# Kernel tuning notes

Hardware: AMD Instinct MI355X
Metric: run time of the kernel (lower is better)

The kernel has to match this reference:

```python
import jax, jax.numpy as jnp
import numpy as np
from jax import lax

BN_EPS = 1e-5

def _bn(x, g, b):
    # eval-mode BatchNorm with default running stats (mean=0, var=1)
    sh = (1, -1) + (1,) * (x.ndim - 2)
    return x * (g / jnp.sqrt(1.0 + BN_EPS)).reshape(sh) + b.reshape(sh)

def _simam(x, lam=1e-4):
    axes = tuple(range(2, x.ndim))
    mu = x.mean(axis=axes, keepdims=True)
    d2 = (x - mu) ** 2
    var = d2.mean(axis=axes, keepdims=True)
    e = d2 / (2.0 * var + 1e-12) + lam
    return jax.nn.sigmoid(1.0 / (e + 1e-12)) * x

def _dwconv1d(x, w, pad, groups):
    return lax.conv_general_dilated(
        x, w, (1,), [(pad, pad)],
        dimension_numbers=('NCH', 'OIH', 'NCH'),
        feature_group_count=groups)

def _adaptive_pool_matrix(t_in, t_out):
    # torch AdaptiveAvgPool1d: window i = [floor(i*t_in/t_out), ceil((i+1)*t_in/t_out))
    M = np.zeros((t_in, t_out), dtype=np.float32)
    for i in range(t_out):
        s = (i * t_in) // t_out
        e = -(-((i + 1) * t_in) // t_out)
        M[s:e, i] = 1.0 / (e - s)
    return jnp.asarray(M)

def _deform_conv1d(x, w, ow, ob):
    # depthwise deformable conv1d, padding='valid'; grid_sample bilinear,
    # zeros padding, align_corners=True -> pure 1D bilinear gather at pos.
    B, C, T = x.shape
    K = w.shape[1]
    T_out = T - K + 1
    off = _dwconv1d(x, ow, 0, C) + ob[None, :, None]        # (B, C*K, T_out)
    off = off.reshape(B, C, K, T_out)
    pos = (jnp.arange(T_out, dtype=x.dtype)[None, None, None, :]
           + jnp.arange(K, dtype=x.dtype)[None, None, :, None] + off)
    i0f = jnp.floor(pos)
    f = pos - i0f
    i0 = i0f.astype(jnp.int32)
    xb = jnp.broadcast_to(x[:, :, None, :], (B, C, K, T))
    def gather(idx):
        valid = (idx >= 0) & (idx < T)
        v = jnp.take_along_axis(xb, jnp.clip(idx, 0, T - 1), axis=3)
        return jnp.where(valid, v, 0.0)
    samp = gather(i0) * (1.0 - f) + gather(i0 + 1) * f      # (B,C,K,T_out)
    return jnp.einsum('bckt,ck->bct', samp, w)

def _branch(x, sw, g1, b1, tw, g2, b2):
    # spatial depthwise conv (kernel covers full channel axis) -> (B,5,T)
    h = jnp.einsum('bcht,ch->bct', x, sw)
    h = _simam(jax.nn.elu(_bn(h, g1, b1)))
    h = _dwconv1d(h, tw, tw.shape[-1] // 2, h.shape[1])     # temporal depthwise, same length
    return _simam(jax.nn.elu(_bn(h, g2, b2)))

def setup_inputs() -> dict:
    key = jax.random.key(0)
    ks = iter(jax.random.split(key, 48))
    B, C_in, T, n_class = 256, 22, 1000, 4
    k1, k2, k3 = 15, 31, 63  # _odd(round(fs*{0.06,0.12,0.25})), fs=250
    def rn(shape, scale=0.1):
        return scale * jax.random.normal(next(ks), shape, dtype=jnp.float32)
    inp = {'x': jax.random.normal(next(ks), (B, 1, C_in, T), dtype=jnp.float32),
           'stem_w': rn((15, 1, 2, 3)),
           'stem_g': 1.0 + rn((15,)), 'stem_b': rn((15,))}
    for i, kt in zip((1, 2, 3), (k1, k2, k3)):
        inp[f'b{i}_sw'] = rn((5, C_in))
        inp[f'b{i}_g1'] = 1.0 + rn((5,)); inp[f'b{i}_b1'] = rn((5,))
        inp[f'b{i}_tw'] = rn((5, 1, kt))
        inp[f'b{i}_g2'] = 1.0 + rn((5,)); inp[f'b{i}_b2'] = rn((5,))
    inp['pw_w'] = rn((5, 15))
    inp['pw_g'] = 1.0 + rn((5,)); inp['pw_b'] = rn((5,))
    inp['d1_w'] = rn((5, 5));  inp['d1_ow'] = rn((25, 1, 5), 0.02);  inp['d1_ob'] = jnp.zeros((25,), jnp.float32)
    inp['d2_w'] = rn((5, 10)); inp['d2_ow'] = rn((50, 1, 10), 0.02); inp['d2_ob'] = jnp.zeros((50,), jnp.float32)
    inp['fc_w'] = rn((n_class, 5 * 25)); inp['fc_b'] = rn((n_class,))
    return inp

def reference(x, stem_w, stem_g, stem_b,
              b1_sw, b1_g1, b1_b1, b1_tw, b1_g2, b1_b2,
              b2_sw, b2_g1, b2_b1, b2_tw, b2_g2, b2_b2,
              b3_sw, b3_g1, b3_b1, b3_tw, b3_g2, b3_b2,
              pw_w, pw_g, pw_b,
              d1_w, d1_ow, d1_ob, d2_w, d2_ow, d2_ob,
              fc_w, fc_b):
    # stem: conv2d k=(2,3) 'same' (torch pads extra on the right for even k)
    h = lax.conv_general_dilated(x, stem_w, (1, 1), [(0, 1), (1, 1)],
                                 dimension_numbers=('NCHW', 'OIHW', 'NCHW'))
    h = jax.nn.elu(_bn(h, stem_g, stem_b))                  # (B,15,22,T); dropout = eval no-op
    o1 = _branch(h[:, 0:5],  b1_sw, b1_g1, b1_b1, b1_tw, b1_g2, b1_b2)
    o2 = _branch(h[:, 5:10], b2_sw, b2_g1, b2_b1, b2_tw, b2_g2, b2_b2)
    o3 = _branch(h[:, 10:15], b3_sw, b3_g1, b3_b1, b3_tw, b3_g2, b3_b2)
    hc = jnp.concatenate([o1, o2, o3], axis=1)              # (B,15,T)
    hc = jnp.einsum('bct,to->bco', hc, _adaptive_pool_matrix(hc.shape[-1], 40))
    hc = jnp.einsum('bct,oc->bot', hc, pw_w)                # 1x1 pointwise
    hc = _simam(jax.nn.elu(_bn(hc, pw_g, pw_b)))            # (B,5,40)
    hc = _deform_conv1d(hc, d1_w, d1_ow, d1_ob)             # (B,5,36)
    hc = _deform_conv1d(hc, d2_w, d2_ow, d2_ob)             # (B,5,27)
    hc = jnp.einsum('bct,to->bco', hc, _adaptive_pool_matrix(hc.shape[-1], 25))
    return hc.reshape(hc.shape[0], -1) @ fc_w.T + fc_b      # (B,n_class)
```

## Files before the change

kernel.cpp:

```cpp
#include <hip/hip_runtime.h>
#include <math.h>

#define BNS 0.99999500003749972f

__device__ __forceinline__ float eluf(float v) {
    return v > 0.f ? v : (__expf(v) - 1.f);
}
__device__ __forceinline__ float sigmf(float u) {
    return 1.f / (1.f + __expf(-u));
}
__device__ __forceinline__ float sgpr(float v) {
    return __int_as_float(__builtin_amdgcn_readfirstlane(__float_as_int(v)));
}

#define PSTR 1024
#define PADZ 32
#define ZLEN 1120

__device__ __forceinline__ void block_reduce2(float& s1, float& s2, float* red) {
#pragma unroll
    for (int m = 32; m > 0; m >>= 1) {
        s1 += __shfl_xor(s1, m, 64);
        s2 += __shfl_xor(s2, m, 64);
    }
    const int wid = threadIdx.x >> 6, lane = threadIdx.x & 63;
    if (lane == 0) { red[wid * 2] = s1; red[wid * 2 + 1] = s2; }
    __syncthreads();
    s1 = red[0] + red[2] + red[4] + red[6];
    s2 = red[1] + red[3] + red[5] + red[7];
}

__global__ __launch_bounds__(256) void k_stem(
    const float* __restrict__ x,
    const float* __restrict__ stem_w,
    const float* __restrict__ stem_g, const float* __restrict__ stem_b,
    const float* __restrict__ sw1, const float* __restrict__ sw2, const float* __restrict__ sw3,
    float* __restrict__ pre)
{
    const int tid = threadIdx.x;
    const int lane = tid & 63;
    const int g = blockIdx.y;
    const int b = blockIdx.z;
    const float* xb = x + b * 22000;

    const float* swp = (g == 0 ? sw1 : g == 1 ? sw2 : sw3);
    float wrow[5];
#pragma unroll
    for (int c = 0; c < 5; ++c)
        wrow[c] = (lane < 22) ? swp[c * 22 + lane] : 0.f;

    if (tid >= 250) return;
    const int t0 = blockIdx.x * 500 + tid * 2;

    float w[5][6], bs[5];
#pragma unroll
    for (int c = 0; c < 5; ++c) {
        const int C = g * 5 + c;
        const float gsc = sgpr(stem_g[C]) * BNS;
#pragma unroll
        for (int j = 0; j < 6; ++j) w[c][j] = sgpr(stem_w[C * 6 + j]) * gsc;
        bs[c] = sgpr(stem_b[C]);
    }

    const bool sel0 = (t0 == 0), sel2 = (t0 == 998);
    const int base = sel0 ? 0 : (sel2 ? 996 : t0 - 1);

    float acc0[5] = {0.f, 0.f, 0.f, 0.f, 0.f};
    float acc1[5] = {0.f, 0.f, 0.f, 0.f, 0.f};

    #define LOADW(rp, w0, w1, w2, w3)                                   \
    {                                                                   \
        const float4 v = *reinterpret_cast<const float4*>((rp) + base); \
        w0 = sel0 ? 0.f : (sel2 ? v.y : v.x);                           \
        w1 = sel0 ? v.x : (sel2 ? v.z : v.y);                           \
        w2 = sel0 ? v.y : (sel2 ? v.w : v.z);                           \
        w3 = sel2 ? 0.f : (sel0 ? v.z : v.w);                           \
    }

    float c0, c1, c2, c3, n0, n1, n2, n3;
    LOADW(xb, c0, c1, c2, c3)
    for (int i = 0; i < 22; ++i) {
        if (i < 21) {
            LOADW(xb + (i + 1) * 1000, n0, n1, n2, n3)
        } else {
            n0 = n1 = n2 = n3 = 0.f;
        }
#pragma unroll
        for (int c = 0; c < 5; ++c) {
            const float sv = __shfl(wrow[c], i, 64);
            float v0 = fmaf(w[c][0], c0, fmaf(w[c][1], c1, fmaf(w[c][2], c2,
                       fmaf(w[c][3], n0, fmaf(w[c][4], n1, fmaf(w[c][5], n2, bs[c]))))));
            float v1 = fmaf(w[c][0], c1, fmaf(w[c][1], c2, fmaf(w[c][2], c3,
                       fmaf(w[c][3], n1, fmaf(w[c][4], n2, fmaf(w[c][5], n3, bs[c]))))));
            acc0[c] += eluf(v0) * sv;
            acc1[c] += eluf(v1) * sv;
        }
        c0 = n0; c1 = n1; c2 = n2; c3 = n3;
    }
    #undef LOADW

    float* prow0 = pre + (b * 15 + g * 5) * PSTR + t0;
#pragma unroll
    for (int c = 0; c < 5; ++c) {
        float2 o; o.x = acc0[c]; o.y = acc1[c];
        *reinterpret_cast<float2*>(prow0 + c * PSTR) = o;
    }
}

template<int K>
__device__ __forceinline__ void branch_block(
    const float* __restrict__ row,
    float g1s, float b1v,
    float wreg,
    float g2s, float b2v,
    float* __restrict__ zrow,
    float* __restrict__ red,
    float* __restrict__ out40)
{
    const int tid = threadIdx.x;
    const int t0 = tid * 4;
    const bool act = tid < 250;

    if (tid < PADZ) zrow[tid] = 0.f;
    if (tid >= 32 && tid < 120) zrow[PADZ + 1000 + (tid - 32)] = 0.f;

    float y0 = 0.f, y1 = 0.f, y2 = 0.f, y3 = 0.f, s1 = 0.f, s2 = 0.f;
    if (act) {
        const float4 v = *reinterpret_cast<const float4*>(row + t0);
        y0 = eluf(v.x * g1s + b1v);
        y1 = eluf(v.y * g1s + b1v);
        y2 = eluf(v.z * g1s + b1v);
        y3 = eluf(v.w * g1s + b1v);
        s1 = y0 + y1 + y2 + y3;
        s2 = y0 * y0 + y1 * y1 + y2 * y2 + y3 * y3;
    }
    block_reduce2(s1, s2, red);
    {
        const float mu = s1 * 1e-3f;
        const float var = s2 * 1e-3f - mu * mu;
        const float iv = 1.f / (2.f * var + 1e-12f);
        if (act) {
            float d;
            float4 z;
            d = y0 - mu; z.x = sigmf(1.f / (d * d * iv + 1e-4f + 1e-12f)) * y0;
            d = y1 - mu; z.y = sigmf(1.f / (d * d * iv + 1e-4f + 1e-12f)) * y1;
            d = y2 - mu; z.z = sigmf(1.f / (d * d * iv + 1e-4f + 1e-12f)) * y2;
            d = y3 - mu; z.w = sigmf(1.f / (d * d * iv + 1e-4f + 1e-12f)) * y3;
            *reinterpret_cast<float4*>(&zrow[PADZ + t0]) = z;
        }
    }
    __syncthreads();

    float a0 = 0.f, a1 = 0.f, a2 = 0.f, a3 = 0.f;
    if (act) {
        const int A = PADZ + t0 - (K / 2) - 1;
        float W[20];
#pragma unroll
        for (int q = 0; q < 5; ++q)
            *reinterpret_cast<float4*>(&W[q * 4]) = *reinterpret_cast<const float4*>(&zrow[A + q * 4]);

#pragma unroll
        for (int cb = 0; cb < K; cb += 16) {
            float P[16];
            if (cb + 16 < K) {
#pragma unroll
                for (int q = 0; q < 4; ++q)
                    *reinterpret_cast<float4*>(&P[q * 4]) =
                        *reinterpret_cast<const float4*>(&zrow[A + cb + 20 + q * 4]);
            }
            const int DD = (K - cb < 16) ? (K - cb) : 16;
#pragma unroll
            for (int dd = 0; dd < DD; ++dd) {
                const float wv = __shfl(wreg, cb + dd, 64);
                a0 += W[dd + 1] * wv;
                a1 += W[dd + 2] * wv;
                a2 += W[dd + 3] * wv;
                a3 += W[dd + 4] * wv;
            }
            if (cb + 16 < K) {
#pragma unroll
                for (int q = 0; q < 4; ++q) W[q] = W[16 + q];
#pragma unroll
                for (int q = 0; q < 16; ++q) W[4 + q] = P[q];
            }
        }
    }

    float u0 = 0.f, u1 = 0.f, u2 = 0.f, u3 = 0.f;
    s1 = 0.f; s2 = 0.f;
    if (act) {
        u0 = eluf(a0 * g2s + b2v);
        u1 = eluf(a1 * g2s + b2v);
        u2 = eluf(a2 * g2s + b2v);
        u3 = eluf(a3 * g2s + b2v);
        s1 = u0 + u1 + u2 + u3;
        s2 = u0 * u0 + u1 * u1 + u2 * u2 + u3 * u3;
    }
    block_reduce2(s1, s2, red);
    {
        const float mu = s1 * 1e-3f;
        const float var = s2 * 1e-3f - mu * mu;
        const float iv = 1.f / (2.f * var + 1e-12f);
        if (act) {
            float d;
            float4 z;
            d = u0 - mu; z.x = sigmf(1.f / (d * d * iv + 1e-4f + 1e-12f)) * u0;
            d = u1 - mu; z.y = sigmf(1.f / (d * d * iv + 1e-4f + 1e-12f)) * u1;
            d = u2 - mu; z.z = sigmf(1.f / (d * d * iv + 1e-4f + 1e-12f)) * u2;
            d = u3 - mu; z.w = sigmf(1.f / (d * d * iv + 1e-4f + 1e-12f)) * u3;
            *reinterpret_cast<float4*>(&zrow[PADZ + t0]) = z;
        }
    }
    __syncthreads();

    if (tid < 40) {
        float s = 0.f;
#pragma unroll
        for (int q = 0; q < 25; ++q) s += zrow[PADZ + tid * 25 + q];
        out40[tid] = s * (1.f / 25.f);
    }
}

__global__ __launch_bounds__(256) void k_branch(
    const float* __restrict__ pre,
    const float* __restrict__ g1a, const float* __restrict__ b1a,
    const float* __restrict__ tw1,
    const float* __restrict__ g2a, const float* __restrict__ b2a,
    const float* __restrict__ g1b, const float* __restrict__ b1b,
    const float* __restrict__ tw2,
    const float* __restrict__ g2b, const float* __restrict__ b2b,
    const float* __restrict__ g1c, const float* __restrict__ b1c,
    const float* __restrict__ tw3,
    const float* __restrict__ g2c, const float* __restrict__ b2c,
    float* __restrict__ pooled)
{
    __shared__ float zrow[ZLEN];
    __shared__ float red[8];

    const int row_id = blockIdx.x;
    const int C = row_id % 15;
    const int br = C / 5, c = C % 5;
    const int lane = threadIdx.x & 63;

    const float* row = pre + (size_t)row_id * PSTR;
    float* out40 = pooled + row_id * 40;

    if (br == 0) {
        const float wreg = (lane < 15) ? tw1[c * 15 + lane] : 0.f;
        branch_block<15>(row, g1a[c] * BNS, b1a[c], wreg, g2a[c] * BNS, b2a[c], zrow, red, out40);
    } else if (br == 1) {
        const float wreg = (lane < 31) ? tw2[c * 31 + lane] : 0.f;
        branch_block<31>(row, g1b[c] * BNS, b1b[c], wreg, g2b[c] * BNS, b2b[c], zrow, red, out40);
    } else {
        const float wreg = (lane < 63) ? tw3[c * 63 + lane] : 0.f;
        branch_block<63>(row, g1c[c] * BNS, b1c[c], wreg, g2c[c] * BNS, b2c[c], zrow, red, out40);
    }
}

__global__ __launch_bounds__(128) void k_head(
    const float* __restrict__ pooled,
    const float* __restrict__ pw_w, const float* __restrict__ pw_g, const float* __restrict__ pw_b,
    const float* __restrict__ d1_w, const float* __restrict__ d1_ow, const float* __restrict__ d1_ob,
    const float* __restrict__ d2_w, const float* __restrict__ d2_ow, const float* __restrict__ d2_ob,
    const float* __restrict__ fc_w, const float* __restrict__ fc_b,
    float* __restrict__ out)
{
    __shared__ float P[600];
    __shared__ float A[200];
    __shared__ float Bv[200];
    __shared__ float C1[180];
    __shared__ float C2[135];
    __shared__ float D[125];
    __shared__ float mu5[5], iv5[5];

    const int b = blockIdx.x, tid = threadIdx.x;

    for (int i = tid; i < 600; i += 128) P[i] = pooled[b * 600 + i];
    __syncthreads();

    for (int i = tid; i < 200; i += 128) {
        int o = i / 40, t = i % 40;
        float s = 0.f;
        for (int cc = 0; cc < 15; ++cc) s += P[cc * 40 + t] * pw_w[o * 15 + cc];
        float v = s * (pw_g[o] * BNS) + pw_b[o];
        A[i] = eluf(v);
    }
    __syncthreads();

    if (tid < 5) {
        float s = 0.f;
        for (int t = 0; t < 40; ++t) s += A[tid * 40 + t];
        float mu = s * (1.f / 40.f);
        float v2 = 0.f;
        for (int t = 0; t < 40; ++t) { float d = A[tid * 40 + t] - mu; v2 += d * d; }
        mu5[tid] = mu;
        iv5[tid] = 1.f / (2.f * (v2 * (1.f / 40.f)) + 1e-12f);
    }
    __syncthreads();

    for (int i = tid; i < 200; i += 128) {
        int o = i / 40;
        float a = A[i];
        float d = a - mu5[o];
        float e = d * d * iv5[o] + 1e-4f;
        Bv[i] = sigmf(1.f / (e + 1e-12f)) * a;
    }
    __syncthreads();

    for (int i = tid; i < 180; i += 128) {
        int cc = i / 36, t = i % 36;
        float o = 0.f;
        for (int k = 0; k < 5; ++k) {
            float off = d1_ob[cc * 5 + k];
            for (int d = 0; d < 5; ++d) off += Bv[cc * 40 + t + d] * d1_ow[(cc * 5 + k) * 5 + d];
            float pos = (float)(t + k) + off;
            float fl = floorf(pos);
            float f = pos - fl;
            int i0 = (int)fl;
            float v0 = (i0 >= 0 && i0 < 40) ? Bv[cc * 40 + i0] : 0.f;
            float v1 = (i0 + 1 >= 0 && i0 + 1 < 40) ? Bv[cc * 40 + i0 + 1] : 0.f;
            o += (v0 * (1.f - f) + v1 * f) * d1_w[cc * 5 + k];
        }
        C1[i] = o;
    }
    __syncthreads();

    for (int i = tid; i < 135; i += 128) {
        int cc = i / 27, t = i % 27;
        float o = 0.f;
        for (int k = 0; k < 10; ++k) {
            float off = d2_ob[cc * 10 + k];
            for (int d = 0; d < 10; ++d) off += C1[cc * 36 + t + d] * d2_ow[(cc * 10 + k) * 10 + d];
            float pos = (float)(t + k) + off;
            float fl = floorf(pos);
            float f = pos - fl;
            int i0 = (int)fl;
            float v0 = (i0 >= 0 && i0 < 36) ? C1[cc * 36 + i0] : 0.f;
            float v1 = (i0 + 1 >= 0 && i0 + 1 < 36) ? C1[cc * 36 + i0 + 1] : 0.f;
            o += (v0 * (1.f - f) + v1 * f) * d2_w[cc * 10 + k];
        }
        C2[i] = o;
    }
    __syncthreads();

    for (int i = tid; i < 125; i += 128) {
        int cc = i / 25, j = i % 25;
        int s0 = (j * 27) / 25;
        int e0 = ((j + 1) * 27 + 24) / 25;
        float s = 0.f;
        for (int q = s0; q < e0; ++q) s += C2[cc * 27 + q];
        D[i] = s / (float)(e0 - s0);
    }
    __syncthreads();

    if (tid < 64) {
        float part0 = 0.f, part1 = 0.f, part2 = 0.f, part3 = 0.f;
        for (int i = tid; i < 125; i += 64) {
            const float dv = D[i];
            part0 += dv * fc_w[0 * 125 + i];
            part1 += dv * fc_w[1 * 125 + i];
            part2 += dv * fc_w[2 * 125 + i];
            part3 += dv * fc_w[3 * 125 + i];
        }
#pragma unroll
        for (int m = 32; m > 0; m >>= 1) {
            part0 += __shfl_xor(part0, m, 64);
            part1 += __shfl_xor(part1, m, 64);
            part2 += __shfl_xor(part2, m, 64);
            part3 += __shfl_xor(part3, m, 64);
        }
        if (tid == 0) {
            out[b * 4 + 0] = part0 + fc_b[0];
            out[b * 4 + 1] = part1 + fc_b[1];
            out[b * 4 + 2] = part2 + fc_b[2];
            out[b * 4 + 3] = part3 + fc_b[3];
        }
    }
}

extern "C" void kernel_launch(void* const* d_in, const int* in_sizes, int n_in,
                              void* d_out, int out_size, void* d_ws, size_t ws_size,
                              hipStream_t stream) {
    const float* x      = (const float*)d_in[0];
    const float* stem_w = (const float*)d_in[1];
    const float* stem_g = (const float*)d_in[2];
    const float* stem_b = (const float*)d_in[3];
    const float* b1_sw = (const float*)d_in[4];
    const float* b1_g1 = (const float*)d_in[5];
    const float* b1_b1 = (const float*)d_in[6];
    const float* b1_tw = (const float*)d_in[7];
    const float* b1_g2 = (const float*)d_in[8];
    const float* b1_b2 = (const float*)d_in[9];
    const float* b2_sw = (const float*)d_in[10];
    const float* b2_g1 = (const float*)d_in[11];
    const float* b2_b1 = (const float*)d_in[12];
    const float* b2_tw = (const float*)d_in[13];
    const float* b2_g2 = (const float*)d_in[14];
    const float* b2_b2 = (const float*)d_in[15];
    const float* b3_sw = (const float*)d_in[16];
    const float* b3_g1 = (const float*)d_in[17];
    const float* b3_b1 = (const float*)d_in[18];
    const float* b3_tw = (const float*)d_in[19];
    const float* b3_g2 = (const float*)d_in[20];
    const float* b3_b2 = (const float*)d_in[21];
    const float* pw_w  = (const float*)d_in[22];
    const float* pw_g  = (const float*)d_in[23];
    const float* pw_b  = (const float*)d_in[24];
    const float* d1_w  = (const float*)d_in[25];
    const float* d1_ow = (const float*)d_in[26];
    const float* d1_ob = (const float*)d_in[27];
    const float* d2_w  = (const float*)d_in[28];
    const float* d2_ow = (const float*)d_in[29];
    const float* d2_ob = (const float*)d_in[30];
    const float* fc_w  = (const float*)d_in[31];
    const float* fc_b  = (const float*)d_in[32];

    float* pre    = (float*)d_ws;
    float* pooled = (float*)((char*)d_ws + (size_t)256 * 15 * PSTR * 4);

    k_stem<<<dim3(2, 3, 256), 256, 0, stream>>>(
        x, stem_w, stem_g, stem_b, b1_sw, b2_sw, b3_sw, pre);

    k_branch<<<3840, 256, 0, stream>>>(
        pre,
        b1_g1, b1_b1, b1_tw, b1_g2, b1_b2,
        b2_g1, b2_b1, b2_tw, b2_g2, b2_b2,
        b3_g1, b3_b1, b3_tw, b3_g2, b3_b2,
        pooled);

    k_head<<<256, 128, 0, stream>>>(
        pooled, pw_w, pw_g, pw_b,
        d1_w, d1_ow, d1_ob, d2_w, d2_ow, d2_ob,
        fc_w, fc_b, (float*)d_out);
}
```

Measured before the change: 75.51 us.

## Fuse head kernel into branch kernel via last-block atomic counter per batch

```diff
diff --git a/kernel.cpp b/kernel.cpp
--- a/kernel.cpp
+++ b/kernel.cpp
@@ -35,13 +35,16 @@
     const float* __restrict__ stem_w,
     const float* __restrict__ stem_g, const float* __restrict__ stem_b,
     const float* __restrict__ sw1, const float* __restrict__ sw2, const float* __restrict__ sw3,
-    float* __restrict__ pre)
+    float* __restrict__ pre,
+    int* __restrict__ counters)
 {
     const int tid = threadIdx.x;
     const int lane = tid & 63;
     const int g = blockIdx.y;
     const int b = blockIdx.z;
     const float* xb = x + b * 22000;
+
+    if (blockIdx.x == 0 && g == 0 && tid == 0) counters[b] = 0;
 
     const float* swp = (g == 0 ? sw1 : g == 1 ? sw2 : sw3);
     float wrow[5];
@@ -106,6 +109,8 @@
         *reinterpret_cast<float2*>(prow0 + c * PSTR) = o;
     }
 }
+
+#define SMEM_F 1460
 
 template<int K>
 __device__ __forceinline__ void branch_block(
@@ -232,15 +237,26 @@
     const float* __restrict__ g1c, const float* __restrict__ b1c,
     const float* __restrict__ tw3,
     const float* __restrict__ g2c, const float* __restrict__ b2c,
-    float* __restrict__ pooled)
+    float* __restrict__ pooled,
+    int* __restrict__ counters,
+    const float* __restrict__ pw_w, const float* __restrict__ pw_g, const float* __restrict__ pw_b,
+    const float* __restrict__ d1_w, const float* __restrict__ d1_ow, const float* __restrict__ d1_ob,
+    const float* __restrict__ d2_w, const float* __restrict__ d2_ow, const float* __restrict__ d2_ob,
+    const float* __restrict__ fc_w, const float* __restrict__ fc_b,
+    float* __restrict__ out)
 {
-    __shared__ float zrow[ZLEN];
-    __shared__ float red[8];
-
+    __shared__ float smem[SMEM_F];
+    __shared__ int is_last;
+
+    const int tid = threadIdx.x;
     const int row_id = blockIdx.x;
+    const int b = row_id / 15;
     const int C = row_id % 15;
     const int br = C / 5, c = C % 5;
-    const int lane = threadIdx.x & 63;
+    const int lane = tid & 63;
+
+    float* zrow = smem;
+    float* red  = smem + 1440;
 
     const float* row = pre + (size_t)row_id * PSTR;
     float* out40 = pooled + row_id * 40;
@@ -255,30 +271,29 @@
         const float wreg = (lane < 63) ? tw3[c * 63 + lane] : 0.f;
         branch_block<63>(row, g1c[c] * BNS, b1c[c], wreg, g2c[c] * BNS, b2c[c], zrow, red, out40);
     }
-}
-
-__global__ __launch_bounds__(128) void k_head(
-    const float* __restrict__ pooled,
-    const float* __restrict__ pw_w, const float* __restrict__ pw_g, const float* __restrict__ pw_b,
-    const float* __restrict__ d1_w, const float* __restrict__ d1_ow, const float* __restrict__ d1_ob,
-    const float* __restrict__ d2_w, const float* __restrict__ d2_ow, const float* __restrict__ d2_ob,
-    const float* __restrict__ fc_w, const float* __restrict__ fc_b,
-    float* __restrict__ out)
-{
-    __shared__ float P[600];
-    __shared__ float A[200];
-    __shared__ float Bv[200];
-    __shared__ float C1[180];
-    __shared__ float C2[135];
-    __shared__ float D[125];
-    __shared__ float mu5[5], iv5[5];
-
-    const int b = blockIdx.x, tid = threadIdx.x;
-
-    for (int i = tid; i < 600; i += 128) P[i] = pooled[b * 600 + i];
-    __syncthreads();
-
-    for (int i = tid; i < 200; i += 128) {
+
+    __syncthreads();
+    if (tid == 0) {
+        __threadfence();
+        is_last = (atomicAdd(&counters[b], 1) == 14);
+    }
+    __syncthreads();
+    if (!is_last) return;
+    __threadfence();
+
+    float* P   = smem;
+    float* A   = smem + 600;
+    float* Bv  = smem + 800;
+    float* C1  = smem + 1000;
+    float* C2  = smem + 1180;
+    float* D   = smem + 1315;
+    float* mu5 = smem + 1440;
+    float* iv5 = smem + 1448;
+
+    for (int i = tid; i < 600; i += 256) P[i] = pooled[b * 600 + i];
+    __syncthreads();
+
+    for (int i = tid; i < 200; i += 256) {
         int o = i / 40, t = i % 40;
         float s = 0.f;
         for (int cc = 0; cc < 15; ++cc) s += P[cc * 40 + t] * pw_w[o * 15 + cc];
@@ -298,7 +313,7 @@
     }
     __syncthreads();
 
-    for (int i = tid; i < 200; i += 128) {
+    for (int i = tid; i < 200; i += 256) {
         int o = i / 40;
         float a = A[i];
         float d = a - mu5[o];
@@ -307,7 +322,7 @@
     }
     __syncthreads();
 
-    for (int i = tid; i < 180; i += 128) {
+    for (int i = tid; i < 180; i += 256) {
         int cc = i / 36, t = i % 36;
         float o = 0.f;
         for (int k = 0; k < 5; ++k) {
@@ -325,7 +340,7 @@
     }
     __syncthreads();
 
-    for (int i = tid; i < 135; i += 128) {
+    for (int i = tid; i < 135; i += 256) {
         int cc = i / 27, t = i % 27;
         float o = 0.f;
         for (int k = 0; k < 10; ++k) {
@@ -343,7 +358,7 @@
     }
     __syncthreads();
 
-    for (int i = tid; i < 125; i += 128) {
+    for (int i = tid; i < 125; i += 256) {
         int cc = i / 25, j = i % 25;
         int s0 = (j * 27) / 25;
         int e0 = ((j + 1) * 27 + 24) / 25;
@@ -415,21 +430,21 @@
     const float* fc_w  = (const float*)d_in[31];
     const float* fc_b  = (const float*)d_in[32];
 
-    float* pre    = (float*)d_ws;
-    float* pooled = (float*)((char*)d_ws + (size_t)256 * 15 * PSTR * 4);
+    float* pre      = (float*)d_ws;
+    float* pooled   = (float*)((char*)d_ws + (size_t)256 * 15 * PSTR * 4);
+    int*   counters = (int*)((char*)d_ws + (size_t)256 * 15 * PSTR * 4
+                                          + (size_t)256 * 15 * 40 * 4);
 
     k_stem<<<dim3(2, 3, 256), 256, 0, stream>>>(
-        x, stem_w, stem_g, stem_b, b1_sw, b2_sw, b3_sw, pre);
+        x, stem_w, stem_g, stem_b, b1_sw, b2_sw, b3_sw, pre, counters);
 
     k_branch<<<3840, 256, 0, stream>>>(
         pre,
         b1_g1, b1_b1, b1_tw, b1_g2, b1_b2,
         b2_g1, b2_b1, b2_tw, b2_g2, b2_b2,
         b3_g1, b3_b1, b3_tw, b3_g2, b3_b2,
-        pooled);
-
-    k_head<<<256, 128, 0, stream>>>(
-        pooled, pw_w, pw_g, pw_b,
+        pooled, counters,
+        pw_w, pw_g, pw_b,
         d1_w, d1_ow, d1_ob, d2_w, d2_ow, d2_ob,
         fc_w, fc_b, (float*)d_out);
 }
```

After: 182.7 us. +142.0%, slower.
